# Performance work log

Hardware: AMD Instinct MI355X
Metric: run time of the kernel (lower is better)

Reference implementation:

```python
import jax, jax.numpy as jnp
import numpy as np
import math

NUM_HEAD = 16
D_MODEL = 1024
BATCH = 2
SEQ = 2048


def setup_inputs() -> dict:
    key = jax.random.key(0)
    k1, k2, k3, k4 = jax.random.split(key, 4)
    scale = 1.0 / math.sqrt(D_MODEL)
    return {
        "query": jax.random.normal(k1, (BATCH, SEQ, D_MODEL), dtype=jnp.float32),
        "key": jax.random.normal(k2, (BATCH, SEQ, D_MODEL), dtype=jnp.float32),
        "value": jax.random.normal(k3, (BATCH, SEQ, D_MODEL), dtype=jnp.float32),
        "w_concat": jax.random.normal(k4, (D_MODEL, D_MODEL), dtype=jnp.float32) * scale,
    }


def _split_heads(x):
    # [B, S, D] -> [B, H, S, d_k]
    B, S, D = x.shape
    return x.reshape(B, S, NUM_HEAD, D // NUM_HEAD).transpose(0, 2, 1, 3)


def reference(query, key, value, w_concat):
    # NOTE: faithful to the source bug — the w_q/w_k/w_v projections are
    # computed then discarded in the original forward; attention runs on the
    # raw (split) inputs.
    q = _split_heads(query)
    k = _split_heads(key)
    v = _split_heads(value)
    d_k = q.shape[-1]
    scores = jnp.einsum("bhqd,bhkd->bhqk", q, k) / math.sqrt(d_k)
    attn = jax.nn.softmax(scores, axis=-1)
    ctx = jnp.einsum("bhqk,bhkd->bhqd", attn, v)
    B, H, S, dk = ctx.shape
    x = ctx.transpose(0, 2, 1, 3).reshape(B, S, H * dk)
    # torch Linear (bias=False): y = x @ W^T
    return x @ w_concat.T
```

## Files before the change

### kernel.cpp

```cpp
#include <hip/hip_runtime.h>

#define BB 2
#define HH 16
#define SS 2048
#define DMODEL 1024

typedef unsigned short ushort_t;
typedef short bf16x8 __attribute__((ext_vector_type(8)));
typedef float f32x4 __attribute__((ext_vector_type(4)));

__device__ __forceinline__ unsigned short f2bf(float f) {
  union { float f; unsigned int u; } x; x.f = f;
  unsigned int u = x.u;
  return (unsigned short)((u + 0x7fffu + ((u >> 16) & 1u)) >> 16);
}
__device__ __forceinline__ unsigned int pack2(float a, float b) {
  return (unsigned int)f2bf(a) | ((unsigned int)f2bf(b) << 16);
}
__device__ __forceinline__ unsigned int cvtpk(float lo, float hi) {
  unsigned int r;
  asm("v_cvt_pk_bf16_f32 %0, %1, %2" : "=v"(r) : "v"(lo), "v"(hi));
  return r;
}
__device__ __forceinline__ void gload16(const ushort_t* g, ushort_t* l) {
  __builtin_amdgcn_global_load_lds(
      (const __attribute__((address_space(1))) void*)g,
      (__attribute__((address_space(3))) void*)l, 16, 0, 0);
}

__global__ void __launch_bounds__(256)
conv_fused(const float* __restrict__ k, const float* __restrict__ v,
           const float* __restrict__ w, ushort_t* __restrict__ Kh,
           ushort_t* __restrict__ Vt, ushort_t* __restrict__ wb) {
  int bid = blockIdx.x;
  int t = threadIdx.x;
  if (bid >= 1024) {
    int i = (bid - 1024) * 256 + t;
    float4 a = *(const float4*)(w + (size_t)i * 8);
    float4 bq = *(const float4*)(w + (size_t)i * 8 + 4);
    uint4 o;
    o.x = pack2(a.x, a.y);
    o.y = pack2(a.z, a.w);
    o.z = pack2(bq.x, bq.y);
    o.w = pack2(bq.z, bq.w);
    *(uint4*)(wb + (size_t)i * 8) = o;
    return;
  }
  const float c_sc = 0.18033688011112042f;
  __shared__ float vlds[64][65];
  int bh = bid >> 5;
  int b = bh >> 4, h = bh & 15;
  int s0 = (bid & 31) * 64;
#pragma unroll
  for (int j = 0; j < 4; ++j) {
    int idx = t + j * 256;
    int r = idx >> 4, c4 = idx & 15;
    size_t in_off = ((size_t)(b * SS + s0 + r)) * DMODEL + h * 64 + c4 * 4;
    float4 ka = *(const float4*)(k + in_off);
    float4 va = *(const float4*)(v + in_off);
    size_t out_off = ((size_t)bh * SS + s0 + r) * 64 + c4 * 4;
    *(uint2*)(Kh + out_off) = make_uint2(pack2(ka.x * c_sc, ka.y * c_sc),
                                         pack2(ka.z * c_sc, ka.w * c_sc));
    vlds[r][c4 * 4 + 0] = va.x;
    vlds[r][c4 * 4 + 1] = va.y;
    vlds[r][c4 * 4 + 2] = va.z;
    vlds[r][c4 * 4 + 3] = va.w;
  }
  __syncthreads();
#pragma unroll
  for (int j = 0; j < 4; ++j) {
    int idx = t + j * 256;
    int d = idx >> 4, u = idx & 15;
    int c = ((u >> 3) << 1) | (u & 1);
    int g = (u >> 1) & 3;
    int m0 = c * 16 + g * 4;
    size_t voff = ((size_t)bh * 64 + d) * SS + s0 + u * 4;
    *(uint2*)(Vt + voff) =
        make_uint2(pack2(vlds[m0 + 0][d], vlds[m0 + 1][d]),
                   pack2(vlds[m0 + 2][d], vlds[m0 + 3][d]));
  }
}

__global__ void __launch_bounds__(512, 1)
attn_fwd(const float* __restrict__ Qsrc, const ushort_t* __restrict__ Kh,
         const ushort_t* __restrict__ Vt, ushort_t* __restrict__ ctx) {
  __shared__ ushort_t K_lds[2][2][64][64];
  __shared__ ushort_t V_lds[2][2][64][64];
  __shared__ __align__(16) float cmb[4][64][84];
  int bid = blockIdx.x;
  int bh = (bid & 7) * 4 + ((bid >> 3) & 3);
  int q0 = (bid >> 5) * 256;
  int b = bh >> 4, h = bh & 15;
  int tid = threadIdx.x;
  int wid = tid >> 6;
  int half = wid >> 2;
  int wq = wid & 3;
  int lane = tid & 63;
  int g = lane >> 4, lr = lane & 15;
  int rsub = lane >> 3, ch = (lane & 7) ^ rsub;

  const ushort_t* Kp = Kh + (size_t)bh * SS * 64;
  const ushort_t* Vp = Vt + (size_t)bh * 64 * SS;

  ushort_t (*Kl)[64][64] = K_lds[half];
  ushort_t (*Vl)[64][64] = V_lds[half];
  const int kvbase = half * (SS / 2);

  auto stage = [&](int buf, int kv) {
#pragma unroll
    for (int j = 0; j < 2; ++j) {
      int i = j * 4 + wq;
      gload16(Kp + (size_t)(kv + i * 8 + rsub) * 64 + ch * 8, &Kl[buf][i * 8][0]);
      gload16(Vp + (size_t)(i * 8 + rsub) * SS + kv + ch * 8, &Vl[buf][i * 8][0]);
    }
  };

  stage(0, kvbase);

  bf16x8 qf[4][2];
#pragma unroll
  for (int qb = 0; qb < 4; ++qb) {
    int row = q0 + wq * 64 + qb * 16 + lr;
    const float* qr = Qsrc + ((size_t)(b * SS + row)) * DMODEL + h * 64;
#pragma unroll
    for (int kk = 0; kk < 2; ++kk) {
      float4 x = *(const float4*)(qr + kk * 32 + g * 8);
      float4 y = *(const float4*)(qr + kk * 32 + g * 8 + 4);
      uint4 wv;
      wv.x = cvtpk(x.x, x.y);
      wv.y = cvtpk(x.z, x.w);
      wv.z = cvtpk(y.x, y.y);
      wv.w = cvtpk(y.z, y.w);
      qf[qb][kk] = *(bf16x8*)&wv;
    }
  }

  const f32x4 vzero = {0.f, 0.f, 0.f, 0.f};
  const short ob = (short)0x3F80;
  const bf16x8 ones = {ob, ob, ob, ob, ob, ob, ob, ob};
  f32x4 o[4][4];
  f32x4 ol[4];
#pragma unroll
  for (int qb = 0; qb < 4; ++qb) {
    ol[qb] = vzero;
#pragma unroll
    for (int d = 0; d < 4; ++d) o[qb][d] = vzero;
  }

  const int NTH = SS / 128;
  auto tile = [&](int cur, int tl) {
    if (tl + 1 < NTH) stage(cur ^ 1, kvbase + (tl + 1) * 64);

    bf16x8 kf[4][2], vf[4][2];
#pragma unroll
    for (int c = 0; c < 4; ++c)
#pragma unroll
      for (int kk = 0; kk < 2; ++kk) {
        kf[c][kk] = *(const bf16x8*)&Kl[cur][c * 16 + lr]
                                       [((kk * 4 + g) ^ (lr & 7)) * 8];
        vf[c][kk] = *(const bf16x8*)&Vl[cur][c * 16 + lr]
                                       [((kk * 4 + g) ^ (lr & 7)) * 8];
      }

#pragma unroll
    for (int qb = 0; qb < 4; ++qb) {
      f32x4 s[4];
      __builtin_amdgcn_s_setprio(1);
#pragma unroll
      for (int c = 0; c < 4; ++c) {
        s[c] = __builtin_amdgcn_mfma_f32_16x16x32_bf16(kf[c][0], qf[qb][0], vzero, 0, 0, 0);
        s[c] = __builtin_amdgcn_mfma_f32_16x16x32_bf16(kf[c][1], qf[qb][1], s[c], 0, 0, 0);
      }
      __builtin_amdgcn_s_setprio(0);
      float p[4][4];
#pragma unroll
      for (int c = 0; c < 4; ++c)
#pragma unroll
        for (int r = 0; r < 4; ++r) p[c][r] = __builtin_amdgcn_exp2f(s[c][r]);
      bf16x8 pf[2];
#pragma unroll
      for (int kk = 0; kk < 2; ++kk) {
        uint4 w;
        w.x = cvtpk(p[kk * 2][0], p[kk * 2][1]);
        w.y = cvtpk(p[kk * 2][2], p[kk * 2][3]);
        w.z = cvtpk(p[kk * 2 + 1][0], p[kk * 2 + 1][1]);
        w.w = cvtpk(p[kk * 2 + 1][2], p[kk * 2 + 1][3]);
        pf[kk] = *(bf16x8*)&w;
      }
      __builtin_amdgcn_s_setprio(1);
      ol[qb] = __builtin_amdgcn_mfma_f32_16x16x32_bf16(pf[0], ones, ol[qb], 0, 0, 0);
      ol[qb] = __builtin_amdgcn_mfma_f32_16x16x32_bf16(pf[1], ones, ol[qb], 0, 0, 0);
#pragma unroll
      for (int d = 0; d < 4; ++d) {
        o[qb][d] = __builtin_amdgcn_mfma_f32_16x16x32_bf16(pf[0], vf[d][0], o[qb][d], 0, 0, 0);
        o[qb][d] = __builtin_amdgcn_mfma_f32_16x16x32_bf16(pf[1], vf[d][1], o[qb][d], 0, 0, 0);
      }
      __builtin_amdgcn_s_setprio(0);
    }
    __syncthreads();
  };

  __syncthreads();
#pragma unroll 1
  for (int tl = 0; tl < NTH; tl += 2) {
    tile(0, tl);
    tile(1, tl + 1);
  }

  if (half) {
#pragma unroll
    for (int qb = 0; qb < 4; ++qb) {
#pragma unroll
      for (int d = 0; d < 4; ++d)
        *(float4*)&cmb[wq][lane][qb * 20 + d * 4] = *(float4*)&o[qb][d];
      *(float4*)&cmb[wq][lane][qb * 20 + 16] = *(float4*)&ol[qb];
    }
  }
  __syncthreads();
  if (!half) {
#pragma unroll
    for (int qb = 0; qb < 4; ++qb) {
      float4 lo = *(float4*)&cmb[wq][lane][qb * 20 + 16];
      float linv[4];
      linv[0] = __builtin_amdgcn_rcpf(ol[qb][0] + lo.x);
      linv[1] = __builtin_amdgcn_rcpf(ol[qb][1] + lo.y);
      linv[2] = __builtin_amdgcn_rcpf(ol[qb][2] + lo.z);
      linv[3] = __builtin_amdgcn_rcpf(ol[qb][3] + lo.w);
#pragma unroll
      for (int d = 0; d < 4; ++d) {
        float4 oo = *(float4*)&cmb[wq][lane][qb * 20 + d * 4];
#pragma unroll
        for (int r = 0; r < 4; ++r) {
          float other = (r == 0) ? oo.x : (r == 1) ? oo.y : (r == 2) ? oo.z : oo.w;
          float val = (o[qb][d][r] + other) * linv[r];
          size_t row = (size_t)b * SS + q0 + wq * 64 + qb * 16 + g * 4 + r;
          ctx[row * DMODEL + h * 64 + d * 16 + lr] = f2bf(val);
        }
      }
    }
  }
}

__global__ void __launch_bounds__(512, 1)
proj_gemm(const ushort_t* __restrict__ A, const ushort_t* __restrict__ Bw,
          float* __restrict__ out) {
  __shared__ ushort_t At[2][128][64];
  __shared__ ushort_t Bt[2][128][64];
  int bid = blockIdx.x;
  int m0 = ((bid & 7) * 4 + ((bid >> 3) & 3)) * 128;
  int n0 = (bid >> 5) * 128;
  int t = threadIdx.x;
  int wid = t >> 6, lane = t & 63;
  int wr = wid >> 2, wc = wid & 3;
  int g = lane >> 4, lr = lane & 15;
  int rsub = lane >> 3, ch = (lane & 7) ^ rsub;
  const f32x4 vzero = {0.f, 0.f, 0.f, 0.f};
  f32x4 acc[4][2];
#pragma unroll
  for (int m = 0; m < 4; ++m)
#pragma unroll
    for (int n = 0; n < 2; ++n) acc[m][n] = vzero;

  auto stage = [&](int buf, int k0) {
#pragma unroll
    for (int j = 0; j < 2; ++j) {
      int i = j * 8 + wid;
      gload16(A + (size_t)(m0 + i * 8 + rsub) * DMODEL + k0 + ch * 8, &At[buf][i * 8][0]);
      gload16(Bw + (size_t)(n0 + i * 8 + rsub) * DMODEL + k0 + ch * 8, &Bt[buf][i * 8][0]);
    }
  };

  const int NTK = DMODEL / 64;
  auto step = [&](int cur, int kt) {
    if (kt + 1 < NTK) stage(cur ^ 1, (kt + 1) * 64);
#pragma unroll
    for (int kk = 0; kk < 2; ++kk) {
      bf16x8 af[4], bf[2];
#pragma unroll
      for (int m = 0; m < 4; ++m)
        af[m] = *(const bf16x8*)&At[cur][wr * 64 + m * 16 + lr]
                                      [((kk * 4 + g) ^ (lr & 7)) * 8];
#pragma unroll
      for (int n = 0; n < 2; ++n)
        bf[n] = *(const bf16x8*)&Bt[cur][wc * 32 + n * 16 + lr]
                                      [((kk * 4 + g) ^ (lr & 7)) * 8];
#pragma unroll
      for (int m = 0; m < 4; ++m)
#pragma unroll
        for (int n = 0; n < 2; ++n)
          acc[m][n] = __builtin_amdgcn_mfma_f32_16x16x32_bf16(af[m], bf[n], acc[m][n], 0, 0, 0);
    }
    __syncthreads();
  };

  stage(0, 0);
  __syncthreads();
#pragma unroll 1
  for (int kt = 0; kt < NTK; kt += 2) {
    step(0, kt);
    step(1, kt + 1);
  }
#pragma unroll
  for (int m = 0; m < 4; ++m)
#pragma unroll
    for (int n = 0; n < 2; ++n)
#pragma unroll
      for (int r = 0; r < 4; ++r)
        out[(size_t)(m0 + wr * 64 + m * 16 + g * 4 + r) * DMODEL +
            n0 + wc * 32 + n * 16 + lr] = acc[m][n][r];
}

extern "C" void kernel_launch(void* const* d_in, const int* in_sizes, int n_in,
                              void* d_out, int out_size, void* d_ws, size_t ws_size,
                              hipStream_t stream) {
  const float* q = (const float*)d_in[0];
  const float* k = (const float*)d_in[1];
  const float* v = (const float*)d_in[2];
  const float* w = (const float*)d_in[3];
  float* out = (float*)d_out;

  size_t nqk = (size_t)BB * HH * SS * 64;
  ushort_t* Kh = (ushort_t*)d_ws;
  ushort_t* Vt = Kh + nqk;
  ushort_t* ctx = Vt + nqk;
  ushort_t* Wb = ctx + (size_t)BB * SS * DMODEL;
  size_t need = (3 * nqk + (size_t)DMODEL * DMODEL) * sizeof(ushort_t);
  if (ws_size < need) return;

  conv_fused<<<1024 + 512, 256, 0, stream>>>(k, v, w, Kh, Vt, Wb);
  attn_fwd<<<256, 512, 0, stream>>>(q, Kh, Vt, ctx);
  proj_gemm<<<256, 512, 0, stream>>>(ctx, Wb, out);
}
```

Measured before the change: 68.63 us.

## Deepen KV LDS pipeline to four buffers with prefetch distance two

Replaces the double-buffered K/V LDS staging with a four-buffer ring that prefetches two tiles ahead. Each tile waits with a partial vmcnt and a barrier instead of a full __syncthreads at the end. The combine scratch buffer is aliased onto the KV LDS region, so total shared memory stays roughly constant. The aim is to hide more global-load latency and cut one barrier per tile, at the cost of relying on a manual vmcnt count that must match the number of outstanding loads.

```diff
diff --git a/kernel.cpp b/kernel.cpp
--- a/kernel.cpp
+++ b/kernel.cpp
@@ -84,9 +84,8 @@
 __global__ void __launch_bounds__(512, 1)
 attn_fwd(const float* __restrict__ Qsrc, const ushort_t* __restrict__ Kh,
          const ushort_t* __restrict__ Vt, ushort_t* __restrict__ ctx) {
-  __shared__ ushort_t K_lds[2][2][64][64];
-  __shared__ ushort_t V_lds[2][2][64][64];
-  __shared__ __align__(16) float cmb[4][64][84];
+  __shared__ __align__(16) ushort_t KV[2][4][2][64][64];
+  float (*cmb)[64][84] = (float(*)[64][84])&KV[0][0][0][0][0];
   int bid = blockIdx.x;
   int bh = (bid & 7) * 4 + ((bid >> 3) & 3);
   int q0 = (bid >> 5) * 256;
@@ -101,21 +100,7 @@
 
   const ushort_t* Kp = Kh + (size_t)bh * SS * 64;
   const ushort_t* Vp = Vt + (size_t)bh * 64 * SS;
-
-  ushort_t (*Kl)[64][64] = K_lds[half];
-  ushort_t (*Vl)[64][64] = V_lds[half];
   const int kvbase = half * (SS / 2);
-
-  auto stage = [&](int buf, int kv) {
-#pragma unroll
-    for (int j = 0; j < 2; ++j) {
-      int i = j * 4 + wq;
-      gload16(Kp + (size_t)(kv + i * 8 + rsub) * 64 + ch * 8, &Kl[buf][i * 8][0]);
-      gload16(Vp + (size_t)(i * 8 + rsub) * SS + kv + ch * 8, &Vl[buf][i * 8][0]);
-    }
-  };
-
-  stage(0, kvbase);
 
   bf16x8 qf[4][2];
 #pragma unroll
@@ -147,21 +132,26 @@
     for (int d = 0; d < 4; ++d) o[qb][d] = vzero;
   }
 
-  const int NTH = SS / 128;
-  auto tile = [&](int cur, int tl) {
-    if (tl + 1 < NTH) stage(cur ^ 1, kvbase + (tl + 1) * 64);
-
+  auto stage = [&](int buf, int kv) {
+#pragma unroll
+    for (int j = 0; j < 2; ++j) {
+      int i = j * 4 + wq;
+      gload16(Kp + (size_t)(kv + i * 8 + rsub) * 64 + ch * 8, &KV[half][buf][0][i * 8][0]);
+      gload16(Vp + (size_t)(i * 8 + rsub) * SS + kv + ch * 8, &KV[half][buf][1][i * 8][0]);
+    }
+  };
+
+  auto computeTile = [&](int cur) {
     bf16x8 kf[4][2], vf[4][2];
 #pragma unroll
     for (int c = 0; c < 4; ++c)
 #pragma unroll
       for (int kk = 0; kk < 2; ++kk) {
-        kf[c][kk] = *(const bf16x8*)&Kl[cur][c * 16 + lr]
+        kf[c][kk] = *(const bf16x8*)&KV[half][cur][0][c * 16 + lr]
                                        [((kk * 4 + g) ^ (lr & 7)) * 8];
-        vf[c][kk] = *(const bf16x8*)&Vl[cur][c * 16 + lr]
+        vf[c][kk] = *(const bf16x8*)&KV[half][cur][1][c * 16 + lr]
                                        [((kk * 4 + g) ^ (lr & 7)) * 8];
       }
-
 #pragma unroll
     for (int qb = 0; qb < 4; ++qb) {
       f32x4 s[4];
@@ -197,15 +187,33 @@
       }
       __builtin_amdgcn_s_setprio(0);
     }
-    __syncthreads();
-  };
+  };
+
+  auto tileW4 = [&](int cur, int tl, int sbuf, bool dostage) {
+    asm volatile("s_waitcnt vmcnt(4)" ::: "memory");
+    __builtin_amdgcn_s_barrier();
+    if (dostage) stage(sbuf, kvbase + (tl + 2) * 64);
+    computeTile(cur);
+  };
+
+  stage(0, kvbase);
+  stage(1, kvbase + 64);
+
+#pragma unroll 1
+  for (int tb = 0; tb < 12; tb += 4) {
+    tileW4(0, tb + 0, 2, true);
+    tileW4(1, tb + 1, 3, true);
+    tileW4(2, tb + 2, 0, true);
+    tileW4(3, tb + 3, 1, true);
+  }
+  tileW4(0, 12, 2, true);
+  tileW4(1, 13, 3, true);
+  tileW4(2, 14, 0, false);
+  asm volatile("s_waitcnt vmcnt(0)" ::: "memory");
+  __builtin_amdgcn_s_barrier();
+  computeTile(3);
 
   __syncthreads();
-#pragma unroll 1
-  for (int tl = 0; tl < NTH; tl += 2) {
-    tile(0, tl);
-    tile(1, tl + 1);
-  }
 
   if (half) {
 #pragma unroll
```

After: 68.48 us (median of 2 runs). No clear change (-0.2%).

## Split attention KV range four ways across 1024-thread blocks

Applied to the files above, without the earlier changes.

Attention blocks grow from 512 to 1024 threads, so the key/value sequence is split into four quarters instead of two, each handled by a group of four waves with its own double-buffered LDS tiles. The combine scratch now reuses the KV LDS buffer. Partial outputs and row sums are reduced through LDS one query block at a time, with barriers between steps. The goal is more waves per CU to hide latency on a grid of 256 blocks; in exchange it adds register pressure under the 1024-thread launch bound and a more serialized reduction with extra barriers.

```diff
diff --git a/kernel.cpp b/kernel.cpp
--- a/kernel.cpp
+++ b/kernel.cpp
@@ -81,19 +81,18 @@
   }
 }
 
-__global__ void __launch_bounds__(512, 1)
+__global__ void __launch_bounds__(1024)
 attn_fwd(const float* __restrict__ Qsrc, const ushort_t* __restrict__ Kh,
          const ushort_t* __restrict__ Vt, ushort_t* __restrict__ ctx) {
-  __shared__ ushort_t K_lds[2][2][64][64];
-  __shared__ ushort_t V_lds[2][2][64][64];
-  __shared__ __align__(16) float cmb[4][64][84];
+  __shared__ __align__(16) ushort_t KV[4][2][2][64][64];
+  float (*cmb)[4][64][21] = (float(*)[4][64][21])&KV[0][0][0][0][0];
   int bid = blockIdx.x;
   int bh = (bid & 7) * 4 + ((bid >> 3) & 3);
   int q0 = (bid >> 5) * 256;
   int b = bh >> 4, h = bh & 15;
   int tid = threadIdx.x;
   int wid = tid >> 6;
-  int half = wid >> 2;
+  int qt = wid >> 2;
   int wq = wid & 3;
   int lane = tid & 63;
   int g = lane >> 4, lr = lane & 15;
@@ -101,17 +100,14 @@
 
   const ushort_t* Kp = Kh + (size_t)bh * SS * 64;
   const ushort_t* Vp = Vt + (size_t)bh * 64 * SS;
-
-  ushort_t (*Kl)[64][64] = K_lds[half];
-  ushort_t (*Vl)[64][64] = V_lds[half];
-  const int kvbase = half * (SS / 2);
+  const int kvbase = qt * (SS / 4);
 
   auto stage = [&](int buf, int kv) {
 #pragma unroll
     for (int j = 0; j < 2; ++j) {
       int i = j * 4 + wq;
-      gload16(Kp + (size_t)(kv + i * 8 + rsub) * 64 + ch * 8, &Kl[buf][i * 8][0]);
-      gload16(Vp + (size_t)(i * 8 + rsub) * SS + kv + ch * 8, &Vl[buf][i * 8][0]);
+      gload16(Kp + (size_t)(kv + i * 8 + rsub) * 64 + ch * 8, &KV[qt][buf][0][i * 8][0]);
+      gload16(Vp + (size_t)(i * 8 + rsub) * SS + kv + ch * 8, &KV[qt][buf][1][i * 8][0]);
     }
   };
 
@@ -147,21 +143,17 @@
     for (int d = 0; d < 4; ++d) o[qb][d] = vzero;
   }
 
-  const int NTH = SS / 128;
-  auto tile = [&](int cur, int tl) {
-    if (tl + 1 < NTH) stage(cur ^ 1, kvbase + (tl + 1) * 64);
-
+  auto computeTile = [&](int cur) {
     bf16x8 kf[4][2], vf[4][2];
 #pragma unroll
     for (int c = 0; c < 4; ++c)
 #pragma unroll
       for (int kk = 0; kk < 2; ++kk) {
-        kf[c][kk] = *(const bf16x8*)&Kl[cur][c * 16 + lr]
+        kf[c][kk] = *(const bf16x8*)&KV[qt][cur][0][c * 16 + lr]
                                        [((kk * 4 + g) ^ (lr & 7)) * 8];
-        vf[c][kk] = *(const bf16x8*)&Vl[cur][c * 16 + lr]
+        vf[c][kk] = *(const bf16x8*)&KV[qt][cur][1][c * 16 + lr]
                                        [((kk * 4 + g) ^ (lr & 7)) * 8];
       }
-
 #pragma unroll
     for (int qb = 0; qb < 4; ++qb) {
       f32x4 s[4];
@@ -197,47 +189,53 @@
       }
       __builtin_amdgcn_s_setprio(0);
     }
+  };
+
+  const int NTQ = SS / 256;
+  auto tile = [&](int cur, int tl) {
+    if (tl + 1 < NTQ) stage(cur ^ 1, kvbase + (tl + 1) * 64);
+    computeTile(cur);
     __syncthreads();
   };
 
   __syncthreads();
 #pragma unroll 1
-  for (int tl = 0; tl < NTH; tl += 2) {
+  for (int tl = 0; tl < NTQ; tl += 2) {
     tile(0, tl);
     tile(1, tl + 1);
   }
 
-  if (half) {
-#pragma unroll
-    for (int qb = 0; qb < 4; ++qb) {
+  __syncthreads();
+#pragma unroll
+  for (int qb = 0; qb < 4; ++qb) {
+    if (qt) {
 #pragma unroll
       for (int d = 0; d < 4; ++d)
-        *(float4*)&cmb[wq][lane][qb * 20 + d * 4] = *(float4*)&o[qb][d];
-      *(float4*)&cmb[wq][lane][qb * 20 + 16] = *(float4*)&ol[qb];
-    }
-  }
-  __syncthreads();
-  if (!half) {
-#pragma unroll
-    for (int qb = 0; qb < 4; ++qb) {
-      float4 lo = *(float4*)&cmb[wq][lane][qb * 20 + 16];
+#pragma unroll
+        for (int r = 0; r < 4; ++r) cmb[qt - 1][wq][lane][d * 4 + r] = o[qb][d][r];
+#pragma unroll
+      for (int r = 0; r < 4; ++r) cmb[qt - 1][wq][lane][16 + r] = ol[qb][r];
+    }
+    __syncthreads();
+    if (!qt) {
       float linv[4];
-      linv[0] = __builtin_amdgcn_rcpf(ol[qb][0] + lo.x);
-      linv[1] = __builtin_amdgcn_rcpf(ol[qb][1] + lo.y);
-      linv[2] = __builtin_amdgcn_rcpf(ol[qb][2] + lo.z);
-      linv[3] = __builtin_amdgcn_rcpf(ol[qb][3] + lo.w);
-#pragma unroll
-      for (int d = 0; d < 4; ++d) {
-        float4 oo = *(float4*)&cmb[wq][lane][qb * 20 + d * 4];
+#pragma unroll
+      for (int r = 0; r < 4; ++r) {
+        float ls = ol[qb][r] + cmb[0][wq][lane][16 + r] +
+                   cmb[1][wq][lane][16 + r] + cmb[2][wq][lane][16 + r];
+        linv[r] = __builtin_amdgcn_rcpf(ls);
+      }
+#pragma unroll
+      for (int d = 0; d < 4; ++d)
 #pragma unroll
         for (int r = 0; r < 4; ++r) {
-          float other = (r == 0) ? oo.x : (r == 1) ? oo.y : (r == 2) ? oo.z : oo.w;
-          float val = (o[qb][d][r] + other) * linv[r];
+          float val = (o[qb][d][r] + cmb[0][wq][lane][d * 4 + r] +
+                       cmb[1][wq][lane][d * 4 + r] + cmb[2][wq][lane][d * 4 + r]) * linv[r];
           size_t row = (size_t)b * SS + q0 + wq * 64 + qb * 16 + g * 4 + r;
           ctx[row * DMODEL + h * 64 + d * 16 + lr] = f2bf(val);
         }
-      }
-    }
+    }
+    __syncthreads();
   }
 }
 
@@ -328,6 +326,6 @@
   if (ws_size < need) return;
 
   conv_fused<<<1024 + 512, 256, 0, stream>>>(k, v, w, Kh, Vt, Wb);
-  attn_fwd<<<256, 512, 0, stream>>>(q, Kh, Vt, ctx);
+  attn_fwd<<<256, 1024, 0, stream>>>(q, Kh, Vt, ctx);
   proj_gemm<<<256, 512, 0, stream>>>(ctx, Wb, out);
 }
```

Result: slower. 267.8 us (+290.2%).
